# Performance work log

Measured on AMD Instinct MI355X. Metric: run time of the kernel, lower is better.

The kernel has to match this reference:

```python
import jax, jax.numpy as jnp
import numpy as np

BS, S, D_IN, D_EMB = 256, 256, 512, 1024
RATIO = 0.3
BN_EPS = 1e-5
VOCAB = 49408


def setup_inputs() -> dict:
    key = jax.random.key(0)
    ks = jax.random.split(key, 12)
    features = jax.random.normal(ks[0], (BS, S, D_IN), dtype=jnp.float32)
    # variable-length token sequences: nonzero ids up to length, 0-padded
    lengths = jax.random.randint(ks[1], (BS,), 3, S + 1)
    tok = jax.random.randint(ks[2], (BS, S), 1, VOCAB)
    text = jnp.where(jnp.arange(S)[None, :] < lengths[:, None], tok, 0).astype(jnp.int32)
    atten = jax.random.normal(ks[3], (BS, S, S), dtype=jnp.float32)
    sc = 0.02
    H = D_EMB // 2  # 512, MLP hidden
    params = {
        "lin_w": jax.random.normal(ks[4], (D_IN, D_EMB), dtype=jnp.float32) * sc,
        "lin_b": jnp.zeros((D_EMB,), dtype=jnp.float32),
        "w1": jax.random.normal(ks[5], (D_IN, H), dtype=jnp.float32) * sc,
        "b1": jnp.zeros((H,), dtype=jnp.float32),
        "g1": jnp.ones((H,), dtype=jnp.float32),
        "be1": jnp.zeros((H,), dtype=jnp.float32),
        "w2": jax.random.normal(ks[6], (H, D_EMB), dtype=jnp.float32) * sc,
        "b2": jnp.zeros((D_EMB,), dtype=jnp.float32),
        "g2": jnp.ones((D_EMB,), dtype=jnp.float32),
        "be2": jnp.zeros((D_EMB,), dtype=jnp.float32),
    }
    return {"features": features, "text": text, "atten": atten, **params}


def _bn_train(x, g, b):
    # BatchNorm1d in train mode: biased batch stats over rows
    m = x.mean(axis=0)
    v = x.var(axis=0)
    return (x - m) * jax.lax.rsqrt(v + BN_EPS) * g + b


def reference(features, text, atten, lin_w, lin_b, w1, b1, g1, be1, w2, b2, g2, be2):
    bs, seq_len = atten.shape[0], atten.shape[1]
    mask = (text != 0).astype(jnp.float32)          # (bs, S)
    token_lens = mask.sum(axis=1)                   # (bs,)
    k = max(1, int((seq_len - 2) * RATIO))          # static
    eos_pos = jnp.clip(token_lens - 1, 0, seq_len - 1).astype(jnp.int32)
    bidx = jnp.arange(bs)
    # scatter writes into atten (faithful to torch in-place updates)
    atten = atten.at[:, :, 0].set(-1.0)
    atten = atten.at[bidx, :, eos_pos].set(-1.0)
    atten = atten.at[bidx, eos_pos, :].set(-1.0)
    atten_sel = atten[bidx, eos_pos, :] * mask      # (bs, S)
    _, topk_idx = jax.lax.top_k(atten_sel, k)       # (bs, k)
    feats_k = jnp.take_along_axis(features, topk_idx[:, :, None], axis=1)  # (bs,k,D_in)
    norm = jnp.maximum(jnp.linalg.norm(feats_k, axis=-1, keepdims=True), 1e-6)
    feats_k = feats_k / norm
    # linear branch
    cap_emb = jnp.einsum("bkd,de->bke", feats_k, lin_w) + lin_b
    # MLP branch: Linear -> BN -> ReLU -> Linear (last layer no BN/ReLU)
    x = feats_k.reshape(bs * k, -1)
    h = jax.nn.relu(_bn_train(x @ w1 + b1, g1, be1))
    o = (h @ w2 + b2).reshape(bs, k, -1)
    fused = o + cap_emb                             # (bs,k,D_emb)
    # maxk_pool1d_var with k=1: max over first pool_lens[i] positions
    pool_lens = jnp.clip(token_lens - 2, 1, k).astype(jnp.int32)
    valid = jnp.arange(k)[None, :] < pool_lens[:, None]  # (bs,k)
    out = jnp.max(jnp.where(valid[:, :, None], fused, -jnp.inf), axis=1)
    return out.astype(jnp.float32)
```

## Files before the change

### kernel.cpp

```cpp
#include <hip/hip_runtime.h>
#include <hip/hip_bf16.h>

typedef __bf16 bf16;
typedef __bf16 bf16x4 __attribute__((ext_vector_type(4)));
typedef __bf16 bf16x8 __attribute__((ext_vector_type(8)));
typedef float  f32x4  __attribute__((ext_vector_type(4)));

#define BSZ   256
#define SEQ   256
#define DIN   512
#define DEMB  1024
#define KSEL  76
#define MROWS (BSZ * KSEL)
#define MTILES (MROWS / 128)
#define PARTQ (MTILES * 512)

__device__ __forceinline__ void gload16(const void* g, void* l) {
  __builtin_amdgcn_global_load_lds((const __attribute__((address_space(1))) void*)g,
                                   (__attribute__((address_space(3))) void*)l, 16, 0, 0);
}

__device__ __forceinline__ unsigned enc(float v) {
  unsigned u = __float_as_uint(v);
  return (u & 0x80000000u) ? ~u : (u | 0x80000000u);
}
__device__ __forceinline__ float dec(unsigned k) {
  return (k & 0x80000000u) ? __uint_as_float(k ^ 0x80000000u) : __uint_as_float(~k);
}

__global__ void k_prep(const int* __restrict__ text, int* __restrict__ topk,
                       int* __restrict__ plen, uint4* __restrict__ keys4) {
  int b = blockIdx.x, t = threadIdx.x;
  keys4[b * 256 + t] = make_uint4(0u, 0u, 0u, 0u);
  __shared__ int red[256];
  red[t] = (text[b * SEQ + t] != 0) ? 1 : 0;
  __syncthreads();
  for (int s = 128; s > 0; s >>= 1) {
    if (t < s) red[t] += red[t + s];
    __syncthreads();
  }
  int len = red[0];
  int z = SEQ - len;
  if (t < KSEL) topk[b * KSEL + t] = (t < z) ? (len + t) : (t - z);
  if (t == 0) {
    int p = len - 2;
    p = p < 1 ? 1 : (p > KSEL ? KSEL : p);
    plen[b] = p;
  }
}

__global__ void k_transpose(const float* __restrict__ W, bf16* __restrict__ Wt,
                            int N, int ldo) {
  __shared__ float tile[32][33];
  int tx = threadIdx.x, ty = threadIdx.y;
  int n = blockIdx.x * 32 + tx;
  int k0 = blockIdx.y * 32;
#pragma unroll
  for (int r = 0; r < 32; r += 8)
    tile[ty + r][tx] = W[(size_t)(k0 + ty + r) * N + n];
  __syncthreads();
#pragma unroll
  for (int r = 0; r < 32; r += 8)
    Wt[(size_t)(blockIdx.x * 32 + ty + r) * ldo + k0 + tx] = (bf16)tile[tx][ty + r];
}

__global__ void k_bias2(const float* __restrict__ a, const float* __restrict__ b,
                        float* __restrict__ o) {
  int i = blockIdx.x * 256 + threadIdx.x;
  o[i] = a[i] + b[i];
}

__global__ void k_gather(const float* __restrict__ feats, const int* __restrict__ topk,
                         bf16* __restrict__ A2) {
  int r = blockIdx.x;
  int b = r / KSEL;
  int src = topk[r];
  const float4* row = (const float4*)(feats + ((size_t)b * SEQ + src) * DIN);
  int t = threadIdx.x;
  float4 v = row[t];
  float ss = v.x * v.x + v.y * v.y + v.z * v.z + v.w * v.w;
#pragma unroll
  for (int o = 32; o > 0; o >>= 1) ss += __shfl_down(ss, o);
  __shared__ float wsum[2];
  if ((t & 63) == 0) wsum[t >> 6] = ss;
  __syncthreads();
  float total = wsum[0] + wsum[1];
  float inv = 1.0f / fmaxf(sqrtf(total), 1e-6f);
  bf16x4 o4;
  o4.x = (bf16)(v.x * inv);
  o4.y = (bf16)(v.y * inv);
  o4.z = (bf16)(v.z * inv);
  o4.w = (bf16)(v.w * inv);
  ((bf16x4*)A2)[(size_t)r * 256 + t] = o4;
}

template<int EPI>
__global__ __launch_bounds__(256, 3)
void k_gemm(const bf16* __restrict__ A, int lda, const bf16* __restrict__ Bt, int ldb,
            const float* __restrict__ bias, bf16* __restrict__ Cb, int ldc, int Kext,
            float* __restrict__ part, const int* __restrict__ plen,
            unsigned* __restrict__ keys) {
  __shared__ __align__(16) bf16 As[128 * 64];
  __shared__ __align__(16) bf16 Bs[128 * 64];
  const int m0 = blockIdx.y * 128, n0 = blockIdx.x * 128;
  const int tid = threadIdx.x, w = tid >> 6, lane = tid & 63;
  const int wr = (w >> 1) * 64, wc = (w & 1) * 64;
  const int srow = lane >> 3;
  const int scol = ((lane & 7) ^ srow) * 8;
  const bf16* Ag = A + (size_t)(m0 + w * 32 + srow) * lda + scol;
  const bf16* Bg = Bt + (size_t)(n0 + w * 32 + srow) * ldb + scol;
  f32x4 acc[4][4] = {};
  const int fr = lane & 15, fg = lane >> 4;
  for (int kt = 0; kt < Kext; kt += 64) {
    __syncthreads();
#pragma unroll
    for (int c = 0; c < 4; ++c) {
      gload16(Ag + (size_t)(c * 8) * lda + kt, &As[(w * 32 + c * 8) * 64]);
      gload16(Bg + (size_t)(c * 8) * ldb + kt, &Bs[(w * 32 + c * 8) * 64]);
    }
    __syncthreads();
#pragma unroll
    for (int kk = 0; kk < 2; ++kk) {
      const int slot = ((kk << 2) | fg) ^ (fr & 7);
      bf16x8 af[4], bfr[4];
#pragma unroll
      for (int i = 0; i < 4; ++i)
        af[i] = *(const bf16x8*)&As[(wr + i * 16 + fr) * 64 + slot * 8];
#pragma unroll
      for (int j = 0; j < 4; ++j)
        bfr[j] = *(const bf16x8*)&Bs[(wc + j * 16 + fr) * 64 + slot * 8];
#pragma unroll
      for (int i = 0; i < 4; ++i)
#pragma unroll
        for (int j = 0; j < 4; ++j)
          acc[i][j] = __builtin_amdgcn_mfma_f32_16x16x32_bf16(af[i], bfr[j], acc[i][j], 0, 0, 0);
    }
  }
  float bv[4];
#pragma unroll
  for (int j = 0; j < 4; ++j) bv[j] = bias[n0 + wc + j * 16 + fr];

  if (EPI == 1) {
    float s[4] = {0, 0, 0, 0}, q[4] = {0, 0, 0, 0};
#pragma unroll
    for (int i = 0; i < 4; ++i)
#pragma unroll
      for (int v = 0; v < 4; ++v) {
        int r = m0 + wr + i * 16 + fg * 4 + v;
        bf16* crow = Cb + (size_t)r * ldc + n0 + wc + fr;
#pragma unroll
        for (int j = 0; j < 4; ++j) {
          float val = acc[i][j][v] + bv[j];
          crow[j * 16] = (bf16)val;
          s[j] += val;
          q[j] += val * val;
        }
      }
#pragma unroll
    for (int j = 0; j < 4; ++j) {
      s[j] += __shfl_down(s[j], 32); s[j] += __shfl_down(s[j], 16);
      q[j] += __shfl_down(q[j], 32); q[j] += __shfl_down(q[j], 16);
    }
    __syncthreads();
    float* red = (float*)As;
    if (lane < 16) {
#pragma unroll
      for (int j = 0; j < 4; ++j) {
        red[(w * 4 + j) * 16 + lane] = s[j];
        red[256 + (w * 4 + j) * 16 + lane] = q[j];
      }
    }
    __syncthreads();
    if (tid < 128) {
      int c = tid;
      int wsel = c >> 6, jj = (c >> 4) & 3, ff = c & 15;
      float ss = red[(wsel * 4 + jj) * 16 + ff] + red[((wsel + 2) * 4 + jj) * 16 + ff];
      float qq = red[256 + (wsel * 4 + jj) * 16 + ff] +
                 red[256 + ((wsel + 2) * 4 + jj) * 16 + ff];
      part[blockIdx.y * 512 + n0 + c] = ss;
      part[PARTQ + blockIdx.y * 512 + n0 + c] = qq;
    }
  } else {
    const float NEG = -__builtin_huge_valf();
    int cur_b = -1, pl = 0;
    bool any = false;
    float cm[4] = {NEG, NEG, NEG, NEG};
#pragma unroll
    for (int i = 0; i < 4; ++i)
#pragma unroll
      for (int v = 0; v < 4; ++v) {
        int gr = m0 + wr + i * 16 + fg * 4 + v;
        int b = gr / KSEL;
        if (b != cur_b) {
          if (any) {
#pragma unroll
            for (int j = 0; j < 4; ++j)
              atomicMax(&keys[(size_t)cur_b * DEMB + n0 + wc + j * 16 + fr], enc(cm[j]));
          }
          cur_b = b;
          pl = plen[b];
          any = false;
#pragma unroll
          for (int j = 0; j < 4; ++j) cm[j] = NEG;
        }
        if (gr - b * KSEL < pl) {
          any = true;
#pragma unroll
          for (int j = 0; j < 4; ++j) cm[j] = fmaxf(cm[j], acc[i][j][v] + bv[j]);
        }
      }
    if (any) {
#pragma unroll
      for (int j = 0; j < 4; ++j)
        atomicMax(&keys[(size_t)cur_b * DEMB + n0 + wc + j * 16 + fr], enc(cm[j]));
    }
  }
}

__global__ void k_bnstats(const float* __restrict__ part, const float* __restrict__ g1,
                          const float* __restrict__ be1, float* __restrict__ bns) {
  int c = threadIdx.x;
  float s = 0, q = 0;
  for (int i = 0; i < MTILES; ++i) {
    s += part[i * 512 + c];
    q += part[PARTQ + i * 512 + c];
  }
  const float invn = 1.0f / (float)MROWS;
  float mean = s * invn;
  float var = q * invn - mean * mean;
  float sc = rsqrtf(var + 1e-5f) * g1[c];
  bns[c] = sc;
  bns[512 + c] = be1[c] - mean * sc;
}

__global__ void k_bnapply(bf16x8* __restrict__ A2v, const float* __restrict__ bns) {
  size_t idx = (size_t)blockIdx.x * 256 + threadIdx.x;
  size_t row = idx >> 6;
  int c = (int)(idx & 63);
  bf16x8* p = A2v + row * 128 + 64 + c;
  bf16x8 v = *p;
  int c8 = c * 8;
  const float4 s0 = *(const float4*)(bns + c8);
  const float4 s1 = *(const float4*)(bns + c8 + 4);
  const float4 h0 = *(const float4*)(bns + 512 + c8);
  const float4 h1 = *(const float4*)(bns + 512 + c8 + 4);
  bf16x8 o;
  o[0] = (bf16)fmaxf(fmaf((float)v[0], s0.x, h0.x), 0.0f);
  o[1] = (bf16)fmaxf(fmaf((float)v[1], s0.y, h0.y), 0.0f);
  o[2] = (bf16)fmaxf(fmaf((float)v[2], s0.z, h0.z), 0.0f);
  o[3] = (bf16)fmaxf(fmaf((float)v[3], s0.w, h0.w), 0.0f);
  o[4] = (bf16)fmaxf(fmaf((float)v[4], s1.x, h1.x), 0.0f);
  o[5] = (bf16)fmaxf(fmaf((float)v[5], s1.y, h1.y), 0.0f);
  o[6] = (bf16)fmaxf(fmaf((float)v[6], s1.z, h1.z), 0.0f);
  o[7] = (bf16)fmaxf(fmaf((float)v[7], s1.w, h1.w), 0.0f);
  *p = o;
}

__global__ void k_decode(const unsigned* __restrict__ keys, float* __restrict__ out) {
  int i = blockIdx.x * 256 + threadIdx.x;
  out[i] = dec(keys[i]);
}

extern "C" void kernel_launch(void* const* d_in, const int* in_sizes, int n_in,
                              void* d_out, int out_size, void* d_ws, size_t ws_size,
                              hipStream_t stream) {
  const float* features = (const float*)d_in[0];
  const int*   text     = (const int*)d_in[1];
  const float* lin_w    = (const float*)d_in[3];
  const float* lin_b    = (const float*)d_in[4];
  const float* w1       = (const float*)d_in[5];
  const float* b1       = (const float*)d_in[6];
  const float* g1       = (const float*)d_in[7];
  const float* be1      = (const float*)d_in[8];
  const float* w2       = (const float*)d_in[9];
  const float* b2       = (const float*)d_in[10];
  float* out = (float*)d_out;
  char* ws = (char*)d_ws;

  int*      topk  = (int*)(ws + 0);
  int*      plen  = (int*)(ws + 77824);
  float*    bns   = (float*)(ws + 78848);
  float*    bias2 = (float*)(ws + 82944);
  float*    part  = (float*)(ws + 87040);
  bf16*     w1t   = (bf16*)(ws + 709632);
  bf16*     b2t   = (bf16*)(ws + 1233920);
  bf16*     A2    = (bf16*)(ws + 3331072);
  unsigned* keys  = (unsigned*)(ws + 43176960);

  k_prep<<<BSZ, 256, 0, stream>>>(text, topk, plen, (uint4*)keys);
  k_transpose<<<dim3(16, 16), dim3(32, 8), 0, stream>>>(w1, w1t, 512, 512);
  k_transpose<<<dim3(32, 16), dim3(32, 8), 0, stream>>>(lin_w, b2t, 1024, 1024);
  k_transpose<<<dim3(32, 16), dim3(32, 8), 0, stream>>>(w2, b2t + 512, 1024, 1024);
  k_bias2<<<4, 256, 0, stream>>>(lin_b, b2, bias2);
  k_gather<<<MROWS, 128, 0, stream>>>(features, topk, A2);
  k_gemm<1><<<dim3(4, MTILES), 256, 0, stream>>>(A2, 1024, w1t, 512, b1, A2 + 512, 1024,
                                                 512, part, nullptr, nullptr);
  k_bnstats<<<1, 512, 0, stream>>>(part, g1, be1, bns);
  k_bnapply<<<4864, 256, 0, stream>>>((bf16x8*)A2, bns);
  k_gemm<2><<<dim3(8, MTILES), 256, 0, stream>>>(A2, 1024, b2t, 1024, bias2, nullptr, 0,
                                                 1024, nullptr, plen, keys);
  k_decode<<<BSZ * DEMB / 256, 256, 0, stream>>>(keys, out);
}
```

Measured before the change: 131.6 us.

## Double-buffer GEMM LDS loads, merge setup kernels, split BN stat reduction

The GEMM main loop now keeps two LDS buffers, so the global-to-LDS load of the next K tile is issued while MFMAs run on the current one. It uses explicit vmcnt waits, raw barriers and raised wave priority around the MFMA block. The LDS doubling lowers launch bounds occupancy from 3 to 2 waves per SIMD. The separate prep, three transpose and bias kernels are merged into one launch to cut launch overhead. The single-block BN stats reduction over 152 tiles is split into a 38-block partial reduction followed by a shorter final pass.

```diff
diff --git a/kernel.cpp b/kernel.cpp
--- a/kernel.cpp
+++ b/kernel.cpp
@@ -14,6 +14,7 @@
 #define MROWS (BSZ * KSEL)
 #define MTILES (MROWS / 128)
 #define PARTQ (MTILES * 512)
+#define NRED  38
 
 __device__ __forceinline__ void gload16(const void* g, void* l) {
   __builtin_amdgcn_global_load_lds((const __attribute__((address_space(1))) void*)g,
@@ -28,46 +29,52 @@
   return (k & 0x80000000u) ? __uint_as_float(k ^ 0x80000000u) : __uint_as_float(~k);
 }
 
-__global__ void k_prep(const int* __restrict__ text, int* __restrict__ topk,
-                       int* __restrict__ plen, uint4* __restrict__ keys4) {
-  int b = blockIdx.x, t = threadIdx.x;
-  keys4[b * 256 + t] = make_uint4(0u, 0u, 0u, 0u);
-  __shared__ int red[256];
-  red[t] = (text[b * SEQ + t] != 0) ? 1 : 0;
-  __syncthreads();
-  for (int s = 128; s > 0; s >>= 1) {
-    if (t < s) red[t] += red[t + s];
+__global__ void k_setup(const int* __restrict__ text, int* __restrict__ topk,
+                        int* __restrict__ plen, uint4* __restrict__ keys4,
+                        const float* __restrict__ w1, bf16* __restrict__ w1t,
+                        const float* __restrict__ lin_w, const float* __restrict__ w2,
+                        bf16* __restrict__ b2t,
+                        const float* __restrict__ lin_b, const float* __restrict__ b2,
+                        float* __restrict__ bias2) {
+  int blk = blockIdx.x, tid = threadIdx.x;
+  if (blk < 256) {
+    int b = blk;
+    keys4[b * 256 + tid] = make_uint4(0u, 0u, 0u, 0u);
+    __shared__ int red[256];
+    red[tid] = (text[b * SEQ + tid] != 0) ? 1 : 0;
     __syncthreads();
-  }
-  int len = red[0];
-  int z = SEQ - len;
-  if (t < KSEL) topk[b * KSEL + t] = (t < z) ? (len + t) : (t - z);
-  if (t == 0) {
-    int p = len - 2;
-    p = p < 1 ? 1 : (p > KSEL ? KSEL : p);
-    plen[b] = p;
-  }
-}
-
-__global__ void k_transpose(const float* __restrict__ W, bf16* __restrict__ Wt,
-                            int N, int ldo) {
-  __shared__ float tile[32][33];
-  int tx = threadIdx.x, ty = threadIdx.y;
-  int n = blockIdx.x * 32 + tx;
-  int k0 = blockIdx.y * 32;
-#pragma unroll
-  for (int r = 0; r < 32; r += 8)
-    tile[ty + r][tx] = W[(size_t)(k0 + ty + r) * N + n];
-  __syncthreads();
-#pragma unroll
-  for (int r = 0; r < 32; r += 8)
-    Wt[(size_t)(blockIdx.x * 32 + ty + r) * ldo + k0 + tx] = (bf16)tile[tx][ty + r];
-}
-
-__global__ void k_bias2(const float* __restrict__ a, const float* __restrict__ b,
-                        float* __restrict__ o) {
-  int i = blockIdx.x * 256 + threadIdx.x;
-  o[i] = a[i] + b[i];
+    for (int s = 128; s > 0; s >>= 1) {
+      if (tid < s) red[tid] += red[tid + s];
+      __syncthreads();
+    }
+    int len = red[0];
+    int z = SEQ - len;
+    if (tid < KSEL) topk[b * KSEL + tid] = (tid < z) ? (len + tid) : (tid - z);
+    if (tid == 0) {
+      int p = len - 2;
+      plen[b] = p < 1 ? 1 : (p > KSEL ? KSEL : p);
+    }
+  } else if (blk < 1536) {
+    const float* W;
+    bf16* Wt;
+    int N, ldo, bx, by;
+    if (blk < 512)       { int t = blk - 256;  W = w1;    Wt = w1t;       N = 512;  ldo = 512;  bx = t & 15; by = t >> 4; }
+    else if (blk < 1024) { int t = blk - 512;  W = lin_w; Wt = b2t;       N = 1024; ldo = 1024; bx = t & 31; by = t >> 5; }
+    else                 { int t = blk - 1024; W = w2;    Wt = b2t + 512; N = 1024; ldo = 1024; bx = t & 31; by = t >> 5; }
+    __shared__ float tile[32][33];
+    int tx = tid & 31, ty = tid >> 5;
+    int n = bx * 32 + tx, k0 = by * 32;
+#pragma unroll
+    for (int r = 0; r < 32; r += 8)
+      tile[ty + r][tx] = W[(size_t)(k0 + ty + r) * N + n];
+    __syncthreads();
+#pragma unroll
+    for (int r = 0; r < 32; r += 8)
+      Wt[(size_t)(bx * 32 + ty + r) * ldo + k0 + tx] = (bf16)tile[tx][ty + r];
+  } else {
+    int i = (blk - 1536) * 256 + tid;
+    bias2[i] = lin_b[i] + b2[i];
+  }
 }
 
 __global__ void k_gather(const float* __restrict__ feats, const int* __restrict__ topk,
@@ -95,13 +102,13 @@
 }
 
 template<int EPI>
-__global__ __launch_bounds__(256, 3)
+__global__ __launch_bounds__(256, 2)
 void k_gemm(const bf16* __restrict__ A, int lda, const bf16* __restrict__ Bt, int ldb,
             const float* __restrict__ bias, bf16* __restrict__ Cb, int ldc, int Kext,
             float* __restrict__ part, const int* __restrict__ plen,
             unsigned* __restrict__ keys) {
-  __shared__ __align__(16) bf16 As[128 * 64];
-  __shared__ __align__(16) bf16 Bs[128 * 64];
+  __shared__ __align__(16) bf16 As[2][128 * 64];
+  __shared__ __align__(16) bf16 Bs[2][128 * 64];
   const int m0 = blockIdx.y * 128, n0 = blockIdx.x * 128;
   const int tid = threadIdx.x, w = tid >> 6, lane = tid & 63;
   const int wr = (w >> 1) * 64, wc = (w & 1) * 64;
@@ -109,33 +116,52 @@
   const int scol = ((lane & 7) ^ srow) * 8;
   const bf16* Ag = A + (size_t)(m0 + w * 32 + srow) * lda + scol;
   const bf16* Bg = Bt + (size_t)(n0 + w * 32 + srow) * ldb + scol;
+  const int nT = Kext >> 6;
   f32x4 acc[4][4] = {};
   const int fr = lane & 15, fg = lane >> 4;
-  for (int kt = 0; kt < Kext; kt += 64) {
-    __syncthreads();
+
+  auto stage = [&](int t, int pb) {
+    const int kt = t << 6;
 #pragma unroll
     for (int c = 0; c < 4; ++c) {
-      gload16(Ag + (size_t)(c * 8) * lda + kt, &As[(w * 32 + c * 8) * 64]);
-      gload16(Bg + (size_t)(c * 8) * ldb + kt, &Bs[(w * 32 + c * 8) * 64]);
-    }
-    __syncthreads();
+      gload16(Ag + (size_t)(c * 8) * lda + kt, &As[pb][(w * 32 + c * 8) * 64]);
+      gload16(Bg + (size_t)(c * 8) * ldb + kt, &Bs[pb][(w * 32 + c * 8) * 64]);
+    }
+  };
+
+  stage(0, 0);
+  for (int t = 0; t < nT; ++t) {
+    const int pb = t & 1;
+    if (t + 1 < nT) {
+      stage(t + 1, pb ^ 1);
+      asm volatile("s_waitcnt vmcnt(8)" ::: "memory");
+    } else {
+      asm volatile("s_waitcnt vmcnt(0)" ::: "memory");
+    }
+    __builtin_amdgcn_s_barrier();
+    __builtin_amdgcn_sched_barrier(0);
 #pragma unroll
     for (int kk = 0; kk < 2; ++kk) {
       const int slot = ((kk << 2) | fg) ^ (fr & 7);
       bf16x8 af[4], bfr[4];
 #pragma unroll
       for (int i = 0; i < 4; ++i)
-        af[i] = *(const bf16x8*)&As[(wr + i * 16 + fr) * 64 + slot * 8];
+        af[i] = *(const bf16x8*)&As[pb][(wr + i * 16 + fr) * 64 + slot * 8];
 #pragma unroll
       for (int j = 0; j < 4; ++j)
-        bfr[j] = *(const bf16x8*)&Bs[(wc + j * 16 + fr) * 64 + slot * 8];
+        bfr[j] = *(const bf16x8*)&Bs[pb][(wc + j * 16 + fr) * 64 + slot * 8];
+      __builtin_amdgcn_s_setprio(1);
 #pragma unroll
       for (int i = 0; i < 4; ++i)
 #pragma unroll
         for (int j = 0; j < 4; ++j)
           acc[i][j] = __builtin_amdgcn_mfma_f32_16x16x32_bf16(af[i], bfr[j], acc[i][j], 0, 0, 0);
-    }
-  }
+      __builtin_amdgcn_s_setprio(0);
+    }
+    asm volatile("s_waitcnt lgkmcnt(0)" ::: "memory");
+    __builtin_amdgcn_s_barrier();
+  }
+
   float bv[4];
 #pragma unroll
   for (int j = 0; j < 4; ++j) bv[j] = bias[n0 + wc + j * 16 + fr];
@@ -162,7 +188,7 @@
       q[j] += __shfl_down(q[j], 32); q[j] += __shfl_down(q[j], 16);
     }
     __syncthreads();
-    float* red = (float*)As;
+    float* red = (float*)&As[0][0];
     if (lane < 16) {
 #pragma unroll
       for (int j = 0; j < 4; ++j) {
@@ -217,13 +243,28 @@
   }
 }
 
-__global__ void k_bnstats(const float* __restrict__ part, const float* __restrict__ g1,
+__global__ void k_bnredA(const float* __restrict__ part, float* __restrict__ part2) {
+  int i = blockIdx.x, t = threadIdx.x;
+  float s0 = 0, s1 = 0, q0 = 0, q1 = 0;
+  for (int j = 0; j < 4; ++j) {
+    const float* p = part + (size_t)(i * 4 + j) * 512 + t * 2;
+    float2 v = *(const float2*)p;
+    float2 u = *(const float2*)(p + PARTQ);
+    s0 += v.x; s1 += v.y; q0 += u.x; q1 += u.y;
+  }
+  part2[i * 512 + t * 2] = s0;
+  part2[i * 512 + t * 2 + 1] = s1;
+  part2[NRED * 512 + i * 512 + t * 2] = q0;
+  part2[NRED * 512 + i * 512 + t * 2 + 1] = q1;
+}
+
+__global__ void k_bnstats(const float* __restrict__ part2, const float* __restrict__ g1,
                           const float* __restrict__ be1, float* __restrict__ bns) {
   int c = threadIdx.x;
   float s = 0, q = 0;
-  for (int i = 0; i < MTILES; ++i) {
-    s += part[i * 512 + c];
-    q += part[PARTQ + i * 512 + c];
+  for (int i = 0; i < NRED; ++i) {
+    s += part2[i * 512 + c];
+    q += part2[NRED * 512 + i * 512 + c];
   }
   const float invn = 1.0f / (float)MROWS;
   float mean = s * invn;
@@ -282,20 +323,19 @@
   float*    bns   = (float*)(ws + 78848);
   float*    bias2 = (float*)(ws + 82944);
   float*    part  = (float*)(ws + 87040);
-  bf16*     w1t   = (bf16*)(ws + 709632);
-  bf16*     b2t   = (bf16*)(ws + 1233920);
-  bf16*     A2    = (bf16*)(ws + 3331072);
-  unsigned* keys  = (unsigned*)(ws + 43176960);
-
-  k_prep<<<BSZ, 256, 0, stream>>>(text, topk, plen, (uint4*)keys);
-  k_transpose<<<dim3(16, 16), dim3(32, 8), 0, stream>>>(w1, w1t, 512, 512);
-  k_transpose<<<dim3(32, 16), dim3(32, 8), 0, stream>>>(lin_w, b2t, 1024, 1024);
-  k_transpose<<<dim3(32, 16), dim3(32, 8), 0, stream>>>(w2, b2t + 512, 1024, 1024);
-  k_bias2<<<4, 256, 0, stream>>>(lin_b, b2, bias2);
+  float*    part2 = (float*)(ws + 709632);
+  bf16*     w1t   = (bf16*)(ws + 865280);
+  bf16*     b2t   = (bf16*)(ws + 1389568);
+  bf16*     A2    = (bf16*)(ws + 3486720);
+  unsigned* keys  = (unsigned*)(ws + 43332608);
+
+  k_setup<<<1540, 256, 0, stream>>>(text, topk, plen, (uint4*)keys,
+                                    w1, w1t, lin_w, w2, b2t, lin_b, b2, bias2);
   k_gather<<<MROWS, 128, 0, stream>>>(features, topk, A2);
   k_gemm<1><<<dim3(4, MTILES), 256, 0, stream>>>(A2, 1024, w1t, 512, b1, A2 + 512, 1024,
                                                  512, part, nullptr, nullptr);
-  k_bnstats<<<1, 512, 0, stream>>>(part, g1, be1, bns);
+  k_bnredA<<<NRED, 256, 0, stream>>>(part, part2);
+  k_bnstats<<<1, 512, 0, stream>>>(part2, g1, be1, bns);
   k_bnapply<<<4864, 256, 0, stream>>>((bf16x8*)A2, bns);
   k_gemm<2><<<dim3(8, MTILES), 256, 0, stream>>>(A2, 1024, b2t, 1024, bias2, nullptr, 0,
                                                  1024, nullptr, plen, keys);
```

New measurement: 133.7 us. No clear change (+1.6%).
